# Optimization experiments

Hardware: AMD Instinct MI355X
Metric: run time of the kernel (lower is better)

Reference implementation:

```python
import jax, jax.numpy as jnp
import numpy as np

HIDDEN = 1024
HEADS = 16
HEAD_DIM = HIDDEN // HEADS
EPS = 1e-5


def setup_inputs() -> dict:
    key = jax.random.key(0)
    ks = jax.random.split(key, 8)
    B, S, D = 2, 2048, HIDDEN
    s = 1.0 / np.sqrt(D)
    return {
        "x": jax.random.normal(ks[0], (B, S, D), dtype=jnp.float32),
        "Wq": jax.random.uniform(ks[1], (D, D), jnp.float32, -s, s),
        "bq": jnp.zeros((D,), jnp.float32),
        "Wk": jax.random.uniform(ks[2], (D, D), jnp.float32, -s, s),
        "bk": jnp.zeros((D,), jnp.float32),
        "Wv": jax.random.uniform(ks[3], (D, D), jnp.float32, -s, s),
        "bv": jnp.zeros((D,), jnp.float32),
        "gamma": jnp.ones((D,), jnp.float32),
        "beta": jnp.zeros((D,), jnp.float32),
    }


def reference(x, Wq, bq, Wk, bk, Wv, bv, gamma, beta):
    B, S, D = x.shape
    H, Hd = HEADS, HEAD_DIM
    # QKV projections -> [B, H, S, Hd]
    q = (x @ Wq + bq).reshape(B, S, H, Hd).transpose(0, 2, 1, 3)
    k = (x @ Wk + bk).reshape(B, S, H, Hd).transpose(0, 2, 1, 3)
    v = (x @ Wv + bv).reshape(B, S, H, Hd).transpose(0, 2, 1, 3)
    scores = jnp.einsum('bhqd,bhkd->bhqk', q, k) / np.sqrt(Hd).astype(np.float32)
    attn = jax.nn.softmax(scores, axis=-1)  # dropout identity in eval
    ctx = jnp.einsum('bhqk,bhkd->bhqd', attn, v)
    ctx = ctx.transpose(0, 2, 1, 3).reshape(B, S, D)
    y = x + ctx
    mu = jnp.mean(y, axis=-1, keepdims=True)
    var = jnp.var(y, axis=-1, keepdims=True)
    out = (y - mu) * jax.lax.rsqrt(var + EPS) * gamma + beta
    return out, attn.mean(axis=1)
```

## Files before the change

### kernel.cpp

```cpp
#include <hip/hip_runtime.h>

#define S_LEN 2048
#define DIM   1024
#define NH    16
#define HD    64

typedef __bf16 bf16x8 __attribute__((ext_vector_type(8)));
typedef __bf16 bf16x4 __attribute__((ext_vector_type(4)));
typedef float  f32x4  __attribute__((ext_vector_type(4)));
typedef float  f32x16 __attribute__((ext_vector_type(16)));
typedef unsigned int u32x4 __attribute__((ext_vector_type(4)));

#define SCALE_Q (0.125f * 1.44269504088896f)

#define GLOAD_LDS16(g, l) __builtin_amdgcn_global_load_lds( \
    (const __attribute__((address_space(1))) void*)(g),     \
    (__attribute__((address_space(3))) void*)(l), 16, 0, 0)

static __device__ __forceinline__ unsigned cvt_pk_bf16(float a, float b) {
  unsigned r;
  asm("v_cvt_pk_bf16_f32 %0, %1, %2" : "=v"(r) : "v"(a), "v"(b));
  return r;
}

__global__ __launch_bounds__(256) void cast_x_kernel(const float* __restrict__ x,
                                                     __bf16* __restrict__ xb) {
  int i = blockIdx.x * 256 + threadIdx.x;
  const float4 a = ((const float4*)x)[i * 2];
  const float4 b = ((const float4*)x)[i * 2 + 1];
  bf16x8 o;
  o[0] = (__bf16)a.x; o[1] = (__bf16)a.y; o[2] = (__bf16)a.z; o[3] = (__bf16)a.w;
  o[4] = (__bf16)b.x; o[5] = (__bf16)b.y; o[6] = (__bf16)b.z; o[7] = (__bf16)b.w;
  ((bf16x8*)xb)[i] = o;
}

__global__ __launch_bounds__(256) void transW_kernel(const float* __restrict__ Wq,
                                                     const float* __restrict__ Wk,
                                                     const float* __restrict__ Wv,
                                                     __bf16* __restrict__ WT) {
  int which = blockIdx.z;
  const float* W = (which == 0) ? Wq : ((which == 1) ? Wk : Wv);
  __bf16* o = WT + (size_t)which * DIM * DIM;
  __shared__ __bf16 t[64][65];
  int k0 = blockIdx.y * 64, n0 = blockIdx.x * 64;
  int tid = threadIdx.x;
  int c4 = (tid & 15) * 4, rb = tid >> 4;
#pragma unroll
  for (int p = 0; p < 4; ++p) {
    int r = p * 16 + rb;
    float4 a = *(const float4*)&W[(size_t)(k0 + r) * DIM + n0 + c4];
    t[r][c4 + 0] = (__bf16)a.x; t[r][c4 + 1] = (__bf16)a.y;
    t[r][c4 + 2] = (__bf16)a.z; t[r][c4 + 3] = (__bf16)a.w;
  }
  __syncthreads();
#pragma unroll
  for (int p = 0; p < 4; ++p) {
    int n = p * 16 + rb;
    bf16x4 v;
    v[0] = t[c4 + 0][n]; v[1] = t[c4 + 1][n];
    v[2] = t[c4 + 2][n]; v[3] = t[c4 + 3][n];
    *(bf16x4*)&o[(size_t)(n0 + n) * DIM + k0 + c4] = v;
  }
}

__global__ __launch_bounds__(256) void qkv_gemm_kernel(const __bf16* __restrict__ xb,
                                                       const __bf16* __restrict__ WT,
                                                       const float* __restrict__ bq,
                                                       const float* __restrict__ bk,
                                                       const float* __restrict__ bv,
                                                       __bf16* __restrict__ qkv) {
  int which = blockIdx.z;
  const __bf16* Wt = WT + (size_t)which * DIM * DIM;
  const float* bias = (which == 0) ? bq : ((which == 1) ? bk : bv);
  __bf16* outp = qkv + (size_t)which * 2 * NH * S_LEN * HD;
  int m0 = blockIdx.y * 128;
  int n0 = blockIdx.x * 128;
  __shared__ __align__(16) char smem[36864];
  __bf16 (*As)[64] = (__bf16(*)[64])smem;
  __bf16 (*Bs)[64] = (__bf16(*)[64])(smem + 16384);
  __bf16 (*Ct)[136] = (__bf16(*)[136])smem;
  int tid = threadIdx.x;
  int wave = tid >> 6, lane = tid & 63;
  int g = lane >> 4, l15 = lane & 15;
  int wm = (wave >> 1) * 64, wn = (wave & 1) * 64;
  int lr = lane >> 3;
  int lc = (lane & 7) * 8;
  const __bf16* ga = &xb[(size_t)(m0 + wave * 32 + lr) * DIM + lc];
  const __bf16* gb = &Wt[(size_t)(n0 + wave * 32 + lr) * DIM + lc];
  f32x4 acc[4][4] = {};
  for (int k0 = 0; k0 < DIM; k0 += 64) {
#pragma unroll
    for (int c = 0; c < 4; ++c) {
      GLOAD_LDS16(ga + k0 + (size_t)(c * 8) * DIM, &As[wave * 32 + c * 8][0]);
      GLOAD_LDS16(gb + k0 + (size_t)(c * 8) * DIM, &Bs[wave * 32 + c * 8][0]);
    }
    __syncthreads();
#pragma unroll
    for (int ks = 0; ks < 2; ++ks) {
      bf16x8 af[4], bfr[4];
#pragma unroll
      for (int s = 0; s < 4; ++s) {
        af[s]  = *(const bf16x8*)&As[wm + s * 16 + l15][ks * 32 + g * 8];
        bfr[s] = *(const bf16x8*)&Bs[wn + s * 16 + l15][ks * 32 + g * 8];
      }
#pragma unroll
      for (int i = 0; i < 4; ++i)
#pragma unroll
        for (int j = 0; j < 4; ++j)
          acc[i][j] = __builtin_amdgcn_mfma_f32_16x16x32_bf16(af[i], bfr[j], acc[i][j], 0, 0, 0);
    }
    __syncthreads();
  }
  if (which != 2) {
    float scale = (which == 0) ? SCALE_Q : 1.0f;
#pragma unroll
    for (int i = 0; i < 4; ++i)
#pragma unroll
      for (int j = 0; j < 4; ++j) {
        int n = n0 + wn + j * 16 + l15;
        float bval = bias[n];
#pragma unroll
        for (int r = 0; r < 4; ++r) {
          int m = m0 + wm + i * 16 + g * 4 + r;
          float val = (acc[i][j][r] + bval) * scale;
          int bb = m >> 11, ss = m & 2047;
          int hh = n >> 6, hd = n & 63;
          outp[(((size_t)bb * NH + hh) * S_LEN + ss) * HD + hd] = (__bf16)val;
        }
      }
  } else {
#pragma unroll
    for (int i = 0; i < 4; ++i)
#pragma unroll
      for (int j = 0; j < 4; ++j) {
        int nl = wn + j * 16 + l15;
        float bval = bias[n0 + nl];
        bf16x4 t;
#pragma unroll
        for (int r = 0; r < 4; ++r) t[r] = (__bf16)(acc[i][j][r] + bval);
        *(bf16x4*)&Ct[nl][wm + i * 16 + g * 4] = t;
      }
    __syncthreads();
#pragma unroll
    for (int it = 0; it < 8; ++it) {
      int idx = (it * 256 + tid) * 8;
      int row = idx >> 7, col = idx & 127;
      int n = n0 + row, hh = n >> 6, hd = n & 63;
      int m = m0 + col, bb = m >> 11, ss = m & 2047;
      *(bf16x8*)&outp[(((size_t)bb * NH + hh) * HD + hd) * S_LEN + ss] =
          *(const bf16x8*)&Ct[row][col];
    }
  }
}

__global__ __launch_bounds__(256) void attn_flash_kernel(const __bf16* __restrict__ qw,
                                                         const __bf16* __restrict__ kw,
                                                         const __bf16* __restrict__ vtw,
                                                         const float* __restrict__ x,
                                                         float* __restrict__ y,
                                                         float* __restrict__ c_out) {
  int qt = blockIdx.x;
  int h  = blockIdx.y;
  int b  = blockIdx.z;
  size_t hoff = (size_t)(b * NH + h) * S_LEN * HD;
  const __bf16* qh = qw + hoff;
  const __bf16* kh = kw + hoff;
  const __bf16* vth = vtw + hoff;
  __shared__ __align__(16) __bf16 Ks[64][64];
  __shared__ __align__(16) __bf16 Vt[64][64];
  int tid = threadIdx.x;
  int wave = tid >> 6, lane = tid & 63;
  int l31 = lane & 31, hi = lane >> 5;
  int swz = (l31 & 7) << 3;
  int q = qt * 128 + wave * 32 + l31;
  bf16x8 qf[4];
#pragma unroll
  for (int ks = 0; ks < 4; ++ks)
    qf[ks] = *(const bf16x8*)&qh[(size_t)q * HD + ks * 16 + hi * 8];
  int sr0 = tid >> 3;
  int sc  = (tid & 7) * 8;
  int swzs = (sr0 & 7) << 3;
  int pl = (sc & 8) ? sc - 4 : sc;
  int ph = (sc & 8) ? sc + 4 : sc + 8;
  float m_r = -1e30f, l_r = 0.f;
  f32x16 ctx0 = {}, ctx1 = {};
  for (int kt = 0; kt < S_LEN / 64; ++kt) {
    __syncthreads();
#pragma unroll
    for (int i = 0; i < 2; ++i) {
      int r = sr0 + i * 32;
      *(bf16x8*)&Ks[r][sc ^ swzs] = *(const bf16x8*)&kh[(size_t)(kt * 64 + r) * HD + sc];
      bf16x8 vv = *(const bf16x8*)&vth[(size_t)r * S_LEN + kt * 64 + sc];
      bf16x4 vlo, vhi4;
#pragma unroll
      for (int e = 0; e < 4; ++e) { vlo[e] = vv[e]; vhi4[e] = vv[e + 4]; }
      *(bf16x4*)&Vt[r][pl ^ swzs] = vlo;
      *(bf16x4*)&Vt[r][ph ^ swzs] = vhi4;
    }
    __syncthreads();
    f32x16 s0 = {}, s1 = {};
#pragma unroll
    for (int ks = 0; ks < 4; ++ks) {
      bf16x8 k0 = *(const bf16x8*)&Ks[l31][(ks * 16 + hi * 8) ^ swz];
      bf16x8 k1 = *(const bf16x8*)&Ks[32 + l31][(ks * 16 + hi * 8) ^ swz];
      s0 = __builtin_amdgcn_mfma_f32_32x32x16_bf16(k0, qf[ks], s0, 0, 0, 0);
      s1 = __builtin_amdgcn_mfma_f32_32x32x16_bf16(k1, qf[ks], s1, 0, 0, 0);
    }
    float vmax = s0[0];
#pragma unroll
    for (int r = 1; r < 16; ++r) vmax = fmaxf(vmax, s0[r]);
#pragma unroll
    for (int r = 0; r < 16; ++r) vmax = fmaxf(vmax, s1[r]);
    vmax = fmaxf(vmax, __shfl_xor(vmax, 32));
    if (__any(vmax > m_r)) {
      float mnew = fmaxf(m_r, vmax);
      float alpha = __builtin_amdgcn_exp2f(m_r - mnew);
      m_r = mnew;
      ctx0 *= alpha; ctx1 *= alpha; l_r *= alpha;
    }
    float ps = 0.f;
#pragma unroll
    for (int r = 0; r < 16; ++r) { s0[r] = __builtin_amdgcn_exp2f(s0[r] - m_r); ps += s0[r]; }
#pragma unroll
    for (int r = 0; r < 16; ++r) { s1[r] = __builtin_amdgcn_exp2f(s1[r] - m_r); ps += s1[r]; }
    ps += __shfl_xor(ps, 32);
    l_r += ps;
    unsigned w[16];
#pragma unroll
    for (int j = 0; j < 8; ++j) w[j]     = cvt_pk_bf16(s0[2 * j], s0[2 * j + 1]);
#pragma unroll
    for (int j = 0; j < 8; ++j) w[8 + j] = cvt_pk_bf16(s1[2 * j], s1[2 * j + 1]);
    bf16x8 pa[4];
#pragma unroll
    for (int f = 0; f < 4; ++f) {
      u32x4 t;
      t[0] = w[f * 4 + 0]; t[1] = w[f * 4 + 1]; t[2] = w[f * 4 + 2]; t[3] = w[f * 4 + 3];
      pa[f] = __builtin_bit_cast(bf16x8, t);
    }
#pragma unroll
    for (int f = 0; f < 4; ++f) {
      bf16x8 v0 = *(const bf16x8*)&Vt[l31][(f * 16 + hi * 8) ^ swz];
      bf16x8 v1 = *(const bf16x8*)&Vt[32 + l31][(f * 16 + hi * 8) ^ swz];
      ctx0 = __builtin_amdgcn_mfma_f32_32x32x16_bf16(v0, pa[f], ctx0, 0, 0, 0);
      ctx1 = __builtin_amdgcn_mfma_f32_32x32x16_bf16(v1, pa[f], ctx1, 0, 0, 0);
    }
  }
  float il = 1.0f / l_r;
  float cvl = m_r + __builtin_amdgcn_logf(l_r);
  if (lane < 32)
    c_out[(size_t)(b * NH + h) * S_LEN + qt * 128 + wave * 32 + lane] = cvl;
  size_t ybase = ((size_t)b * S_LEN + q) * DIM + h * HD;
#pragma unroll
  for (int rq = 0; rq < 4; ++rq) {
    int hd0 = rq * 8 + hi * 4;
    float4 xv0 = *(const float4*)&x[ybase + hd0];
    float4 o0;
    o0.x = xv0.x + ctx0[rq * 4 + 0] * il;
    o0.y = xv0.y + ctx0[rq * 4 + 1] * il;
    o0.z = xv0.z + ctx0[rq * 4 + 2] * il;
    o0.w = xv0.w + ctx0[rq * 4 + 3] * il;
    *(float4*)&y[ybase + hd0] = o0;
    int hd1 = 32 + hd0;
    float4 xv1 = *(const float4*)&x[ybase + hd1];
    float4 o1;
    o1.x = xv1.x + ctx1[rq * 4 + 0] * il;
    o1.y = xv1.y + ctx1[rq * 4 + 1] * il;
    o1.z = xv1.z + ctx1[rq * 4 + 2] * il;
    o1.w = xv1.w + ctx1[rq * 4 + 3] * il;
    *(float4*)&y[ybase + hd1] = o1;
  }
}

__global__ __launch_bounds__(256) void attn_mean_kernel(const __bf16* __restrict__ qw,
                                                        const __bf16* __restrict__ kw,
                                                        const float* __restrict__ c_in,
                                                        float* __restrict__ out_mean) {
  int kt = blockIdx.x, qt = blockIdx.y, b = blockIdx.z;
  __shared__ __align__(16) __bf16 Ks[64][64];
  int tid = threadIdx.x;
  int wave = tid >> 6, lane = tid & 63;
  int l31 = lane & 31, hi = lane >> 5;
  int swz = (l31 & 7) << 3;
  int q = qt * 128 + wave * 32 + l31;
  const __bf16* qp = qw + (size_t)b * NH * S_LEN * HD;
  const __bf16* kp = kw + (size_t)b * NH * S_LEN * HD;
  int sr0 = tid >> 3;
  int sc  = (tid & 7) * 8;
  int swzs = (sr0 & 7) << 3;
  f32x16 macc0 = {}, macc1 = {};
  for (int h = 0; h < NH; ++h) {
    size_t hb = (size_t)h * S_LEN * HD;
    __syncthreads();
#pragma unroll
    for (int i = 0; i < 2; ++i) {
      int r = sr0 + i * 32;
      *(bf16x8*)&Ks[r][sc ^ swzs] = *(const bf16x8*)&kp[hb + (size_t)(kt * 64 + r) * HD + sc];
    }
    __syncthreads();
    f32x16 s0 = {}, s1 = {};
#pragma unroll
    for (int ks = 0; ks < 4; ++ks) {
      bf16x8 qfr = *(const bf16x8*)&qp[hb + (size_t)q * HD + ks * 16 + hi * 8];
      bf16x8 k0 = *(const bf16x8*)&Ks[l31][(ks * 16 + hi * 8) ^ swz];
      bf16x8 k1 = *(const bf16x8*)&Ks[32 + l31][(ks * 16 + hi * 8) ^ swz];
      s0 = __builtin_amdgcn_mfma_f32_32x32x16_bf16(k0, qfr, s0, 0, 0, 0);
      s1 = __builtin_amdgcn_mfma_f32_32x32x16_bf16(k1, qfr, s1, 0, 0, 0);
    }
    float c = c_in[(size_t)(b * NH + h) * S_LEN + q];
#pragma unroll
    for (int r = 0; r < 16; ++r) macc0[r] += __builtin_amdgcn_exp2f(s0[r] - c);
#pragma unroll
    for (int r = 0; r < 16; ++r) macc1[r] += __builtin_amdgcn_exp2f(s1[r] - c);
  }
  const float invh = 1.0f / (float)NH;
  size_t obase = ((size_t)b * S_LEN + q) * S_LEN + kt * 64;
#pragma unroll
  for (int rq = 0; rq < 4; ++rq) {
    int k0i = rq * 8 + hi * 4;
    float4 o0;
    o0.x = macc0[rq * 4 + 0] * invh; o0.y = macc0[rq * 4 + 1] * invh;
    o0.z = macc0[rq * 4 + 2] * invh; o0.w = macc0[rq * 4 + 3] * invh;
    *(float4*)&out_mean[obase + k0i] = o0;
    float4 o1;
    o1.x = macc1[rq * 4 + 0] * invh; o1.y = macc1[rq * 4 + 1] * invh;
    o1.z = macc1[rq * 4 + 2] * invh; o1.w = macc1[rq * 4 + 3] * invh;
    *(float4*)&out_mean[obase + 32 + k0i] = o1;
  }
}

__global__ __launch_bounds__(256) void ln_kernel(const float* __restrict__ y,
                                                 const float* __restrict__ gamma,
                                                 const float* __restrict__ beta,
                                                 float* __restrict__ out) {
  int row = blockIdx.x;
  const float* yr = y + (size_t)row * DIM;
  int tid = threadIdx.x;
  float4 v = *(const float4*)&yr[tid * 4];
  float s = v.x + v.y + v.z + v.w;
  float sq = v.x * v.x + v.y * v.y + v.z * v.z + v.w * v.w;
#pragma unroll
  for (int off = 1; off < 64; off <<= 1) {
    s += __shfl_xor(s, off);
    sq += __shfl_xor(sq, off);
  }
  __shared__ float red[8];
  int wave = tid >> 6, lane = tid & 63;
  if (lane == 0) { red[wave] = s; red[4 + wave] = sq; }
  __syncthreads();
  s = red[0] + red[1] + red[2] + red[3];
  sq = red[4] + red[5] + red[6] + red[7];
  float mu = s * (1.0f / DIM);
  float var = sq * (1.0f / DIM) - mu * mu;
  float rstd = rsqrtf(var + 1e-5f);
  float* orow = out + (size_t)row * DIM;
  float4 gv = *(const float4*)&gamma[tid * 4];
  float4 bv = *(const float4*)&beta[tid * 4];
  float4 ov;
  ov.x = (v.x - mu) * rstd * gv.x + bv.x;
  ov.y = (v.y - mu) * rstd * gv.y + bv.y;
  ov.z = (v.z - mu) * rstd * gv.z + bv.z;
  ov.w = (v.w - mu) * rstd * gv.w + bv.w;
  *(float4*)&orow[tid * 4] = ov;
}

extern "C" void kernel_launch(void* const* d_in, const int* in_sizes, int n_in,
                              void* d_out, int out_size, void* d_ws, size_t ws_size,
                              hipStream_t stream) {
  const float* x  = (const float*)d_in[0];
  const float* Wq = (const float*)d_in[1];
  const float* bq = (const float*)d_in[2];
  const float* Wk = (const float*)d_in[3];
  const float* bk = (const float*)d_in[4];
  const float* Wv = (const float*)d_in[5];
  const float* bv = (const float*)d_in[6];
  const float* gamma = (const float*)d_in[7];
  const float* beta  = (const float*)d_in[8];
  float* out = (float*)d_out;

  char* ws = (char*)d_ws;
  __bf16* xb   = (__bf16*)ws;
  __bf16* WT   = (__bf16*)(ws + 8388608);
  __bf16* qkv  = (__bf16*)(ws + 14680064);
  float*  y    = (float*)(ws + 39845888);
  float*  c_ws = (float*)(ws + 56623104);

  cast_x_kernel<<<2048, 256, 0, stream>>>(x, xb);
  transW_kernel<<<dim3(16, 16, 3), 256, 0, stream>>>(Wq, Wk, Wv, WT);
  qkv_gemm_kernel<<<dim3(8, 32, 3), 256, 0, stream>>>(xb, WT, bq, bk, bv, qkv);
  attn_flash_kernel<<<dim3(16, 16, 2), 256, 0, stream>>>(qkv, qkv + 4194304, qkv + 8388608,
                                                         x, y, c_ws);
  attn_mean_kernel<<<dim3(32, 16, 2), 256, 0, stream>>>(qkv, qkv + 4194304, c_ws,
                                                        out + 4194304);
  ln_kernel<<<4096, 256, 0, stream>>>(y, gamma, beta, out);
}
```

Baseline: 195.6 us.

## Split flash attention KV loop across two wave groups and prefetch tiles

The flash attention kernel now runs 512 threads per block. Two halves of 4 waves each process alternating 64-key tiles, and their partial softmax states and context accumulators are merged through shared memory at the end. Register prefetch of the next K/V tile and s_setprio around the MFMA sections are added to overlap global loads with compute. The attention-mean kernel also prefetches the next head's K tile and hoists its Q fragment loads. This doubles the waves per block to hide latency, at the cost of more LDS, an extra merge step, and higher register pressure under the 512-thread, min-4-blocks launch bound.

Result: faster. 181.3 us (-7.3%).

```diff
diff --git a/kernel.cpp b/kernel.cpp
--- a/kernel.cpp
+++ b/kernel.cpp
@@ -153,12 +153,12 @@
   }
 }
 
-__global__ __launch_bounds__(256) void attn_flash_kernel(const __bf16* __restrict__ qw,
-                                                         const __bf16* __restrict__ kw,
-                                                         const __bf16* __restrict__ vtw,
-                                                         const float* __restrict__ x,
-                                                         float* __restrict__ y,
-                                                         float* __restrict__ c_out) {
+__global__ __launch_bounds__(512, 4) void attn_flash_kernel(const __bf16* __restrict__ qw,
+                                                            const __bf16* __restrict__ kw,
+                                                            const __bf16* __restrict__ vtw,
+                                                            const float* __restrict__ x,
+                                                            float* __restrict__ y,
+                                                            float* __restrict__ c_out) {
   int qt = blockIdx.x;
   int h  = blockIdx.y;
   int b  = blockIdx.z;
@@ -166,46 +166,74 @@
   const __bf16* qh = qw + hoff;
   const __bf16* kh = kw + hoff;
   const __bf16* vth = vtw + hoff;
-  __shared__ __align__(16) __bf16 Ks[64][64];
-  __shared__ __align__(16) __bf16 Vt[64][64];
+  __shared__ __align__(16) char smem[33792];
+  __bf16 (*Ks)[64] = (__bf16(*)[64])smem;
+  __bf16 (*Vt)[64] = (__bf16(*)[64])(smem + 16384);
+  float (*ctxbuf)[64] = (float(*)[64])smem;
+  float* mlbuf = (float*)(smem + 32768);
   int tid = threadIdx.x;
   int wave = tid >> 6, lane = tid & 63;
+  int half = wave >> 2, wsub = wave & 3;
   int l31 = lane & 31, hi = lane >> 5;
   int swz = (l31 & 7) << 3;
-  int q = qt * 128 + wave * 32 + l31;
+  int q = qt * 128 + wsub * 32 + l31;
+  int qlocal = wsub * 32 + l31;
+  __bf16 (*Ksh)[64] = Ks + half * 64;
+  __bf16 (*Vth)[64] = Vt + half * 64;
   bf16x8 qf[4];
 #pragma unroll
   for (int ks = 0; ks < 4; ++ks)
     qf[ks] = *(const bf16x8*)&qh[(size_t)q * HD + ks * 16 + hi * 8];
-  int sr0 = tid >> 3;
-  int sc  = (tid & 7) * 8;
+  int st = tid & 255;
+  int sr0 = st >> 3;
+  int sc  = (st & 7) * 8;
   int swzs = (sr0 & 7) << 3;
   int pl = (sc & 8) ? sc - 4 : sc;
   int ph = (sc & 8) ? sc + 4 : sc + 8;
+  bf16x8 kv[2], vv[2];
+  {
+    int kt0 = half;
+#pragma unroll
+    for (int i = 0; i < 2; ++i) {
+      int r = sr0 + i * 32;
+      kv[i] = *(const bf16x8*)&kh[(size_t)(kt0 * 64 + r) * HD + sc];
+      vv[i] = *(const bf16x8*)&vth[(size_t)r * S_LEN + kt0 * 64 + sc];
+    }
+  }
   float m_r = -1e30f, l_r = 0.f;
   f32x16 ctx0 = {}, ctx1 = {};
-  for (int kt = 0; kt < S_LEN / 64; ++kt) {
+  for (int t = 0; t < 16; ++t) {
     __syncthreads();
 #pragma unroll
     for (int i = 0; i < 2; ++i) {
       int r = sr0 + i * 32;
-      *(bf16x8*)&Ks[r][sc ^ swzs] = *(const bf16x8*)&kh[(size_t)(kt * 64 + r) * HD + sc];
-      bf16x8 vv = *(const bf16x8*)&vth[(size_t)r * S_LEN + kt * 64 + sc];
+      *(bf16x8*)&Ksh[r][sc ^ swzs] = kv[i];
       bf16x4 vlo, vhi4;
 #pragma unroll
-      for (int e = 0; e < 4; ++e) { vlo[e] = vv[e]; vhi4[e] = vv[e + 4]; }
-      *(bf16x4*)&Vt[r][pl ^ swzs] = vlo;
-      *(bf16x4*)&Vt[r][ph ^ swzs] = vhi4;
+      for (int e = 0; e < 4; ++e) { vlo[e] = vv[i][e]; vhi4[e] = vv[i][e + 4]; }
+      *(bf16x4*)&Vth[r][pl ^ swzs] = vlo;
+      *(bf16x4*)&Vth[r][ph ^ swzs] = vhi4;
+    }
+    if (t < 15) {
+      int ktn = 2 * (t + 1) + half;
+#pragma unroll
+      for (int i = 0; i < 2; ++i) {
+        int r = sr0 + i * 32;
+        kv[i] = *(const bf16x8*)&kh[(size_t)(ktn * 64 + r) * HD + sc];
+        vv[i] = *(const bf16x8*)&vth[(size_t)r * S_LEN + ktn * 64 + sc];
+      }
     }
     __syncthreads();
     f32x16 s0 = {}, s1 = {};
+    __builtin_amdgcn_s_setprio(1);
 #pragma unroll
     for (int ks = 0; ks < 4; ++ks) {
-      bf16x8 k0 = *(const bf16x8*)&Ks[l31][(ks * 16 + hi * 8) ^ swz];
-      bf16x8 k1 = *(const bf16x8*)&Ks[32 + l31][(ks * 16 + hi * 8) ^ swz];
+      bf16x8 k0 = *(const bf16x8*)&Ksh[l31][(ks * 16 + hi * 8) ^ swz];
+      bf16x8 k1 = *(const bf16x8*)&Ksh[32 + l31][(ks * 16 + hi * 8) ^ swz];
       s0 = __builtin_amdgcn_mfma_f32_32x32x16_bf16(k0, qf[ks], s0, 0, 0, 0);
       s1 = __builtin_amdgcn_mfma_f32_32x32x16_bf16(k1, qf[ks], s1, 0, 0, 0);
     }
+    __builtin_amdgcn_s_setprio(0);
     float vmax = s0[0];
 #pragma unroll
     for (int r = 1; r < 16; ++r) vmax = fmaxf(vmax, s0[r]);
@@ -225,49 +253,78 @@
     for (int r = 0; r < 16; ++r) { s1[r] = __builtin_amdgcn_exp2f(s1[r] - m_r); ps += s1[r]; }
     ps += __shfl_xor(ps, 32);
     l_r += ps;
-    unsigned w[16];
-#pragma unroll
-    for (int j = 0; j < 8; ++j) w[j]     = cvt_pk_bf16(s0[2 * j], s0[2 * j + 1]);
-#pragma unroll
-    for (int j = 0; j < 8; ++j) w[8 + j] = cvt_pk_bf16(s1[2 * j], s1[2 * j + 1]);
     bf16x8 pa[4];
 #pragma unroll
+    for (int f = 0; f < 2; ++f) {
+      u32x4 tt;
+#pragma unroll
+      for (int j = 0; j < 4; ++j) tt[j] = cvt_pk_bf16(s0[f * 8 + 2 * j], s0[f * 8 + 2 * j + 1]);
+      pa[f] = __builtin_bit_cast(bf16x8, tt);
+    }
+#pragma unroll
+    for (int f = 0; f < 2; ++f) {
+      u32x4 tt;
+#pragma unroll
+      for (int j = 0; j < 4; ++j) tt[j] = cvt_pk_bf16(s1[f * 8 + 2 * j], s1[f * 8 + 2 * j + 1]);
+      pa[2 + f] = __builtin_bit_cast(bf16x8, tt);
+    }
+    __builtin_amdgcn_s_setprio(1);
+#pragma unroll
     for (int f = 0; f < 4; ++f) {
-      u32x4 t;
-      t[0] = w[f * 4 + 0]; t[1] = w[f * 4 + 1]; t[2] = w[f * 4 + 2]; t[3] = w[f * 4 + 3];
-      pa[f] = __builtin_bit_cast(bf16x8, t);
-    }
-#pragma unroll
-    for (int f = 0; f < 4; ++f) {
-      bf16x8 v0 = *(const bf16x8*)&Vt[l31][(f * 16 + hi * 8) ^ swz];
-      bf16x8 v1 = *(const bf16x8*)&Vt[32 + l31][(f * 16 + hi * 8) ^ swz];
+      bf16x8 v0 = *(const bf16x8*)&Vth[l31][(f * 16 + hi * 8) ^ swz];
+      bf16x8 v1 = *(const bf16x8*)&Vth[32 + l31][(f * 16 + hi * 8) ^ swz];
       ctx0 = __builtin_amdgcn_mfma_f32_32x32x16_bf16(v0, pa[f], ctx0, 0, 0, 0);
       ctx1 = __builtin_amdgcn_mfma_f32_32x32x16_bf16(v1, pa[f], ctx1, 0, 0, 0);
     }
-  }
-  float il = 1.0f / l_r;
-  float cvl = m_r + __builtin_amdgcn_logf(l_r);
-  if (lane < 32)
-    c_out[(size_t)(b * NH + h) * S_LEN + qt * 128 + wave * 32 + lane] = cvl;
-  size_t ybase = ((size_t)b * S_LEN + q) * DIM + h * HD;
-#pragma unroll
-  for (int rq = 0; rq < 4; ++rq) {
-    int hd0 = rq * 8 + hi * 4;
-    float4 xv0 = *(const float4*)&x[ybase + hd0];
-    float4 o0;
-    o0.x = xv0.x + ctx0[rq * 4 + 0] * il;
-    o0.y = xv0.y + ctx0[rq * 4 + 1] * il;
-    o0.z = xv0.z + ctx0[rq * 4 + 2] * il;
-    o0.w = xv0.w + ctx0[rq * 4 + 3] * il;
-    *(float4*)&y[ybase + hd0] = o0;
-    int hd1 = 32 + hd0;
-    float4 xv1 = *(const float4*)&x[ybase + hd1];
-    float4 o1;
-    o1.x = xv1.x + ctx1[rq * 4 + 0] * il;
-    o1.y = xv1.y + ctx1[rq * 4 + 1] * il;
-    o1.z = xv1.z + ctx1[rq * 4 + 2] * il;
-    o1.w = xv1.w + ctx1[rq * 4 + 3] * il;
-    *(float4*)&y[ybase + hd1] = o1;
+    __builtin_amdgcn_s_setprio(0);
+  }
+  __syncthreads();
+  int sw2 = (qlocal & 7) << 2;
+  if (half == 1) {
+#pragma unroll
+    for (int rq = 0; rq < 4; ++rq) {
+      int hd0 = rq * 8 + hi * 4;
+      f32x4 a, bb;
+#pragma unroll
+      for (int j = 0; j < 4; ++j) { a[j] = ctx0[rq * 4 + j]; bb[j] = ctx1[rq * 4 + j]; }
+      *(f32x4*)&ctxbuf[qlocal][hd0 ^ sw2] = a;
+      *(f32x4*)&ctxbuf[qlocal][(32 + hd0) ^ sw2] = bb;
+    }
+    if (hi == 0) { mlbuf[qlocal] = m_r; mlbuf[128 + qlocal] = l_r; }
+  }
+  __syncthreads();
+  if (half == 0) {
+    float m1 = mlbuf[qlocal], l1 = mlbuf[128 + qlocal];
+    float m = fmaxf(m_r, m1);
+    float a0 = __builtin_amdgcn_exp2f(m_r - m);
+    float a1 = __builtin_amdgcn_exp2f(m1 - m);
+    float l = a0 * l_r + a1 * l1;
+    float il = 1.0f / l;
+    float cvl = m + __builtin_amdgcn_logf(l);
+    if (lane < 32)
+      c_out[(size_t)(b * NH + h) * S_LEN + qt * 128 + wsub * 32 + lane] = cvl;
+    size_t ybase = ((size_t)b * S_LEN + q) * DIM + h * HD;
+#pragma unroll
+    for (int rq = 0; rq < 4; ++rq) {
+      int hd0 = rq * 8 + hi * 4;
+      f32x4 c1 = *(const f32x4*)&ctxbuf[qlocal][hd0 ^ sw2];
+      float4 xv0 = *(const float4*)&x[ybase + hd0];
+      float4 o0;
+      o0.x = xv0.x + (a0 * ctx0[rq * 4 + 0] + a1 * c1[0]) * il;
+      o0.y = xv0.y + (a0 * ctx0[rq * 4 + 1] + a1 * c1[1]) * il;
+      o0.z = xv0.z + (a0 * ctx0[rq * 4 + 2] + a1 * c1[2]) * il;
+      o0.w = xv0.w + (a0 * ctx0[rq * 4 + 3] + a1 * c1[3]) * il;
+      *(float4*)&y[ybase + hd0] = o0;
+      int hd1 = 32 + hd0;
+      f32x4 c2 = *(const f32x4*)&ctxbuf[qlocal][hd1 ^ sw2];
+      float4 xv1 = *(const float4*)&x[ybase + hd1];
+      float4 o1;
+      o1.x = xv1.x + (a0 * ctx1[rq * 4 + 0] + a1 * c2[0]) * il;
+      o1.y = xv1.y + (a0 * ctx1[rq * 4 + 1] + a1 * c2[1]) * il;
+      o1.z = xv1.z + (a0 * ctx1[rq * 4 + 2] + a1 * c2[2]) * il;
+      o1.w = xv1.w + (a0 * ctx1[rq * 4 + 3] + a1 * c2[3]) * il;
+      *(float4*)&y[ybase + hd1] = o1;
+    }
   }
 }
 
@@ -287,25 +344,38 @@
   int sr0 = tid >> 3;
   int sc  = (tid & 7) * 8;
   int swzs = (sr0 & 7) << 3;
+  bf16x8 kv[2];
+#pragma unroll
+  for (int i = 0; i < 2; ++i)
+    kv[i] = *(const bf16x8*)&kp[(size_t)(kt * 64 + sr0 + i * 32) * HD + sc];
   f32x16 macc0 = {}, macc1 = {};
   for (int h = 0; h < NH; ++h) {
     size_t hb = (size_t)h * S_LEN * HD;
-    __syncthreads();
-#pragma unroll
-    for (int i = 0; i < 2; ++i) {
-      int r = sr0 + i * 32;
-      *(bf16x8*)&Ks[r][sc ^ swzs] = *(const bf16x8*)&kp[hb + (size_t)(kt * 64 + r) * HD + sc];
+    bf16x8 qfr[4];
+#pragma unroll
+    for (int ks = 0; ks < 4; ++ks)
+      qfr[ks] = *(const bf16x8*)&qp[hb + (size_t)q * HD + ks * 16 + hi * 8];
+    __syncthreads();
+#pragma unroll
+    for (int i = 0; i < 2; ++i)
+      *(bf16x8*)&Ks[sr0 + i * 32][sc ^ swzs] = kv[i];
+    if (h < NH - 1) {
+      size_t hbn = (size_t)(h + 1) * S_LEN * HD;
+#pragma unroll
+      for (int i = 0; i < 2; ++i)
+        kv[i] = *(const bf16x8*)&kp[hbn + (size_t)(kt * 64 + sr0 + i * 32) * HD + sc];
     }
     __syncthreads();
     f32x16 s0 = {}, s1 = {};
+    __builtin_amdgcn_s_setprio(1);
 #pragma unroll
     for (int ks = 0; ks < 4; ++ks) {
-      bf16x8 qfr = *(const bf16x8*)&qp[hb + (size_t)q * HD + ks * 16 + hi * 8];
       bf16x8 k0 = *(const bf16x8*)&Ks[l31][(ks * 16 + hi * 8) ^ swz];
       bf16x8 k1 = *(const bf16x8*)&Ks[32 + l31][(ks * 16 + hi * 8) ^ swz];
-      s0 = __builtin_amdgcn_mfma_f32_32x32x16_bf16(k0, qfr, s0, 0, 0, 0);
-      s1 = __builtin_amdgcn_mfma_f32_32x32x16_bf16(k1, qfr, s1, 0, 0, 0);
-    }
+      s0 = __builtin_amdgcn_mfma_f32_32x32x16_bf16(k0, qfr[ks], s0, 0, 0, 0);
+      s1 = __builtin_amdgcn_mfma_f32_32x32x16_bf16(k1, qfr[ks], s1, 0, 0, 0);
+    }
+    __builtin_amdgcn_s_setprio(0);
     float c = c_in[(size_t)(b * NH + h) * S_LEN + q];
 #pragma unroll
     for (int r = 0; r < 16; ++r) macc0[r] += __builtin_amdgcn_exp2f(s0[r] - c);
@@ -387,7 +457,7 @@
   cast_x_kernel<<<2048, 256, 0, stream>>>(x, xb);
   transW_kernel<<<dim3(16, 16, 3), 256, 0, stream>>>(Wq, Wk, Wv, WT);
   qkv_gemm_kernel<<<dim3(8, 32, 3), 256, 0, stream>>>(xb, WT, bq, bk, bv, qkv);
-  attn_flash_kernel<<<dim3(16, 16, 2), 256, 0, stream>>>(qkv, qkv + 4194304, qkv + 8388608,
+  attn_flash_kernel<<<dim3(16, 16, 2), 512, 0, stream>>>(qkv, qkv + 4194304, qkv + 8388608,
                                                          x, y, c_ws);
   attn_mean_kernel<<<dim3(32, 16, 2), 256, 0, stream>>>(qkv, qkv + 4194304, c_ws,
                                                         out + 4194304);
```
